# Performance work log

Hardware: AMD Instinct MI355X
Metric: run time of the kernel (lower is better)

The kernel has to match this reference:

```python
import jax, jax.numpy as jnp
import numpy as np

B, L, F = 16, 1080, 2
D = 128          # d_model
NC = 64          # num_cnn_channels
DIN = 256        # expand * d_model
N = 16           # d_state
K = 4            # d_conv
R = 8            # dt_rank = ceil(d_model/16)
OUT = 3
NB = 3           # num_mamba_blocks


def setup_inputs() -> dict:
    key = jax.random.key(0)
    ks = jax.random.split(key, 24)
    nrm = lambda k, shape, s=0.05: (jax.random.normal(k, shape) * s).astype(jnp.float32)
    bn = lambda c: jnp.stack([jnp.ones(c), jnp.zeros(c), jnp.zeros(c), jnp.ones(c)]).astype(jnp.float32)
    return {
        'x': jax.random.normal(ks[0], (B, L, F), dtype=jnp.float32),
        'emb_W': nrm(ks[1], (F, D), 0.5), 'emb_b': jnp.zeros(D, jnp.float32),
        'c3_W': nrm(ks[2], (NC, D, 3)), 'c3_b': jnp.zeros(NC, jnp.float32), 'bn3': bn(NC),
        'c5_W': nrm(ks[3], (NC, D, 5)), 'c5_b': jnp.zeros(NC, jnp.float32), 'bn5': bn(NC),
        'c7_W': nrm(ks[4], (NC, D, 7)), 'c7_b': jnp.zeros(NC, jnp.float32), 'bn7': bn(NC),
        'cf_W': nrm(ks[5], (D, 3 * NC, 1)), 'cf_b': jnp.zeros(D, jnp.float32), 'bnf': bn(D),
        'ln_g': jnp.ones((NB, D), jnp.float32), 'ln_b': jnp.zeros((NB, D), jnp.float32),
        'in_W': nrm(ks[6], (NB, 2 * DIN, D)),
        'mconv_W': nrm(ks[7], (NB, DIN, K), 0.2), 'mconv_b': jnp.zeros((NB, DIN), jnp.float32),
        'xproj_W': nrm(ks[8], (NB, R + 2 * N, DIN)),
        'dt_W': nrm(ks[9], (NB, DIN, R), 0.1), 'dt_b': jnp.full((NB, DIN), -1.0, jnp.float32),
        'A_log': jnp.tile(jnp.log(jnp.arange(1.0, N + 1.0, dtype=jnp.float32)), (NB, DIN, 1)),
        'Dp': jnp.ones((NB, DIN), jnp.float32),
        'out_W': nrm(ks[10], (NB, D, DIN)),
        'flin_W': nrm(ks[11], (D, 2 * D)), 'flin_b': jnp.zeros(D, jnp.float32),
        'fc_W': nrm(ks[12], (OUT, D)), 'fc_b': jnp.zeros(OUT, jnp.float32),
    }


def conv1d(x, W, b, pad):
    # x: (B,C,L), W: (O,C,K)
    y = jax.lax.conv_general_dilated(x, W, (1,), [(pad, pad)],
                                     dimension_numbers=('NCH', 'OIH', 'NCH'))
    return y + b[None, :, None]


def bn_relu(x, bn, eps=1e-5):
    g, b, m, v = bn  # each (C,)
    return jax.nn.relu((x - m[None, :, None]) * (g / jnp.sqrt(v + eps))[None, :, None] + b[None, :, None])


def layernorm(x, g, b, eps=1e-5):
    mu = x.mean(-1, keepdims=True)
    var = ((x - mu) ** 2).mean(-1, keepdims=True)
    return (x - mu) / jnp.sqrt(var + eps) * g + b


def pos_encoding(seq_len, d_model):
    pos = jnp.arange(seq_len, dtype=jnp.float32)[:, None]
    div = jnp.exp(jnp.arange(0, d_model, 2, dtype=jnp.float32) * (-np.log(10000.0) / d_model))
    pe = jnp.zeros((seq_len, d_model), jnp.float32)
    pe = pe.at[:, 0::2].set(jnp.sin(pos * div)).at[:, 1::2].set(jnp.cos(pos * div))
    return pe


def selective_scan(u, dt, A, Bm, Cm, Dp):
    # u,dt: (b,l,d); A: (d,n); Bm,Cm: (b,l,n); Dp: (d,)
    dA = jnp.exp(dt[..., None] * A)                    # (b,l,d,n)
    dBu = (dt * u)[..., None] * Bm[:, :, None, :]      # (b,l,d,n)

    def step(h, t):
        dA_t, dBu_t, C_t = t
        h = dA_t * h + dBu_t                           # (b,d,n)
        return h, jnp.einsum('bdn,bn->bd', h, C_t)

    h0 = jnp.zeros((u.shape[0], u.shape[2], A.shape[1]), u.dtype)
    _, ys = jax.lax.scan(step, h0, (jnp.swapaxes(dA, 0, 1), jnp.swapaxes(dBu, 0, 1), jnp.swapaxes(Cm, 0, 1)))
    return jnp.swapaxes(ys, 0, 1) + u * Dp


def mamba_block(x, in_W, conv_W, conv_b, xproj_W, dt_W, dt_b, A_log, Dp, out_W):
    xz = x @ in_W.T                                    # (b,l,2*din)
    xs, z = jnp.split(xz, 2, axis=-1)
    xc = jnp.swapaxes(xs, 1, 2)                        # (b,din,l)
    xc = jax.lax.conv_general_dilated(xc, conv_W[:, None, :], (1,), [(K - 1, 0)],
                                      dimension_numbers=('NCH', 'OIH', 'NCH'),
                                      feature_group_count=DIN)
    u = jax.nn.silu(jnp.swapaxes(xc + conv_b[None, :, None], 1, 2))  # (b,l,din)
    dbl = u @ xproj_W.T
    dt, Bm, Cm = dbl[..., :R], dbl[..., R:R + N], dbl[..., R + N:]
    dt = jax.nn.softplus(dt @ dt_W.T + dt_b)
    A = -jnp.exp(A_log)
    y = selective_scan(u, dt, A, Bm, Cm, Dp)
    return (y * jax.nn.silu(z)) @ out_W.T


def reference(x, emb_W, emb_b, c3_W, c3_b, bn3, c5_W, c5_b, bn5, c7_W, c7_b, bn7,
              cf_W, cf_b, bnf, ln_g, ln_b, in_W, mconv_W, mconv_b, xproj_W,
              dt_W, dt_b, A_log, Dp, out_W, flin_W, flin_b, fc_W, fc_b):
    xe = x @ emb_W + emb_b + pos_encoding(x.shape[1], emb_W.shape[1])  # (B,L,D)
    ci = jnp.swapaxes(xe, 1, 2)                                        # (B,D,L)
    o3 = bn_relu(conv1d(ci, c3_W, c3_b, 1), bn3)
    o5 = bn_relu(conv1d(ci, c5_W, c5_b, 2), bn5)
    o7 = bn_relu(conv1d(ci, c7_W, c7_b, 3), bn7)
    cc = jnp.concatenate([o3, o5, o7], axis=1)                         # (B,3*NC,L)
    cf = bn_relu(conv1d(cc, cf_W, cf_b, 0), bnf)
    cnn_feat = jnp.swapaxes(cf, 1, 2)                                  # (B,L,D)
    m = xe
    for i in range(NB):  # Sequential(LN, Mamba, Dropout) -- no residual, dropout=eval
        m = mamba_block(layernorm(m, ln_g[i], ln_b[i]), in_W[i], mconv_W[i], mconv_b[i],
                        xproj_W[i], dt_W[i], dt_b[i], A_log[i], Dp[i], out_W[i])
    fused = jax.nn.relu(jnp.concatenate([cnn_feat, m], axis=-1) @ flin_W.T + flin_b)
    pooled = fused.mean(axis=1)                                        # AdaptiveAvgPool1d(1)
    return pooled @ fc_W.T + fc_b
```

## Files before the change

### kernel.cpp

```cpp
#include <hip/hip_runtime.h>
#include <math.h>

#define LSEQ   1080
#define NBATCH 16
#define BLROWS (LSEQ*NBATCH)
#define CHN    27
#define LCH    40

typedef __bf16  bf16x8 __attribute__((ext_vector_type(8)));
typedef float   f32x4  __attribute__((ext_vector_type(4)));
typedef short   short8 __attribute__((ext_vector_type(8)));
typedef short   short4v __attribute__((ext_vector_type(4)));

__device__ __forceinline__ float silu_f(float x) { return x / (1.f + __expf(-x)); }

__device__ __forceinline__ unsigned short f2bf(float f) {
    unsigned int u = __float_as_uint(f);
    u += 0x7fffu + ((u >> 16) & 1u);
    return (unsigned short)(u >> 16);
}
__device__ __forceinline__ float bf2f(unsigned short h) {
    return __uint_as_float(((unsigned int)h) << 16);
}

__global__ __launch_bounds__(256) void embed_kernel(
    const float* __restrict__ x, const float* __restrict__ embW,
    const float* __restrict__ embb, float* __restrict__ xe)
{
    int idx = blockIdx.x * 256 + threadIdx.x;
    if (idx >= BLROWS * 128) return;
    int d = idx & 127;
    int r = idx >> 7;
    int t = r % LSEQ;
    float x0 = x[(size_t)r * 2], x1 = x[(size_t)r * 2 + 1];
    int i2 = d & 126;
    float div = expf((float)i2 * (-9.210340371976184f / 128.f));
    float arg = (float)t * div;
    float pe = (d & 1) ? cosf(arg) : sinf(arg);
    xe[idx] = fmaf(x0, embW[d], fmaf(x1, embW[128 + d], embb[d] + pe));
}

__global__ __launch_bounds__(256) void convw_all(
    const float* __restrict__ c3W, const float* __restrict__ c5W,
    const float* __restrict__ c7W, const float* __restrict__ cfW,
    const float* __restrict__ inW, const float* __restrict__ xpW,
    const float* __restrict__ otW, const float* __restrict__ flW,
    unsigned short* __restrict__ c3h, unsigned short* __restrict__ c3l,
    unsigned short* __restrict__ c5h, unsigned short* __restrict__ c5l,
    unsigned short* __restrict__ c7h, unsigned short* __restrict__ c7l,
    unsigned short* __restrict__ cfh, unsigned short* __restrict__ cfl,
    unsigned short* __restrict__ inh, unsigned short* __restrict__ inl,
    unsigned short* __restrict__ xph, unsigned short* __restrict__ xpl,
    unsigned short* __restrict__ oth, unsigned short* __restrict__ otl,
    unsigned short* __restrict__ flh, unsigned short* __restrict__ fll)
{
    int idx = blockIdx.x * 256 + threadIdx.x;
    float v;
    unsigned short *dh, *dl;
    int off;
    if (idx < 122880) {
        const float* src; int T;
        if (idx < 24576)      { src = c3W; T = 3; off = idx;          dh = c3h; dl = c3l; }
        else if (idx < 65536) { src = c5W; T = 5; off = idx - 24576;  dh = c5h; dl = c5l; }
        else                  { src = c7W; T = 7; off = idx - 65536;  dh = c7h; dl = c7l; }
        int kk = off % (128 * T);
        int n  = off / (128 * T);
        int tap = kk / 128, d = kk % 128;
        v = src[((size_t)n * 128 + d) * T + tap];
    } else if (idx < 147456) {
        off = idx - 122880; dh = cfh; dl = cfl; v = cfW[off];
    } else if (idx < 344064) {
        off = idx - 147456; dh = inh; dl = inl; v = inW[off];
    } else if (idx < 393216) {
        off = idx - 344064; dh = xph; dl = xpl;
        int k = off % 256;
        int n = (off / 256) % 64;
        int blk = off / (256 * 64);
        v = (n < 40) ? xpW[((size_t)blk * 40 + n) * 256 + k] : 0.f;
    } else if (idx < 491520) {
        off = idx - 393216; dh = oth; dl = otl; v = otW[off];
    } else {
        off = idx - 491520; dh = flh; dl = fll; v = flW[off];
    }
    unsigned short h = f2bf(v);
    dh[off] = h;
    dl[off] = f2bf(v - bf2f(h));
}

template<int BM, int BN>
__device__ __forceinline__ void gemm_body(
    const float* __restrict__ Ab, int lda,
    const unsigned short* __restrict__ Wh, const unsigned short* __restrict__ Wl,
    int Ntot, int Kd, int KT, int pad,
    const float* __restrict__ bias, const float* __restrict__ bn, int bnN, int epi,
    float* __restrict__ Cb, int ldc, int t0, int n0)
{
    constexpr int WM = BM / 2, WN = BN / 2;
    constexpr int MR = WM / 16, NR = WN / 16;
    constexpr int LA = (BM * 8) / 256;
    constexpr int LB = (BN * 4) / 256;

    __shared__ unsigned short Ah[BM][40], Al[BM][40];
    __shared__ unsigned short Bh[BN][40], Bl[BN][40];

    const int tid = threadIdx.x;
    const int wrow = Kd * KT;
    const int lane = tid & 63, wid = tid >> 6;
    const int wr = wid >> 1, wc = wid & 1;
    const int fr = lane & 15, fq = lane >> 4;

    f32x4 acc[MR][NR];
#pragma unroll
    for (int m = 0; m < MR; ++m)
#pragma unroll
        for (int n = 0; n < NR; ++n) acc[m][n] = (f32x4){0.f, 0.f, 0.f, 0.f};

    for (int tap = 0; tap < KT; ++tap) {
        const int shift = tap - pad;
        for (int ks = 0; ks < Kd; ks += 32) {
#pragma unroll
            for (int l = 0; l < LA; ++l) {
                int c = tid + l * 256;
                int row = c >> 3, kc = (c & 7) << 2;
                int ts = t0 + row + shift;
                float4 av = make_float4(0.f, 0.f, 0.f, 0.f);
                if (ts >= 0 && ts < LSEQ)
                    av = *(const float4*)(Ab + (size_t)ts * lda + ks + kc);
                alignas(8) unsigned short hs[4], ls[4];
                float fv[4] = {av.x, av.y, av.z, av.w};
#pragma unroll
                for (int j = 0; j < 4; ++j) {
                    unsigned short h = f2bf(fv[j]);
                    hs[j] = h;
                    ls[j] = f2bf(fv[j] - bf2f(h));
                }
                *(short4v*)&Ah[row][kc] = *(short4v*)hs;
                *(short4v*)&Al[row][kc] = *(short4v*)ls;
            }
            const int kglob = tap * Kd + ks;
#pragma unroll
            for (int l = 0; l < LB; ++l) {
                int c = tid + l * 256;
                int col = c >> 2, kc = (c & 3) << 3;
                size_t src = (size_t)(n0 + col) * wrow + kglob + kc;
                *(short8*)&Bh[col][kc] = *(const short8*)&Wh[src];
                *(short8*)&Bl[col][kc] = *(const short8*)&Wl[src];
            }
            __syncthreads();
            bf16x8 bhf[NR], blf[NR];
#pragma unroll
            for (int n = 0; n < NR; ++n) {
                int colr = wc * WN + n * 16 + fr;
                bhf[n] = __builtin_bit_cast(bf16x8, *(const short8*)&Bh[colr][fq * 8]);
                blf[n] = __builtin_bit_cast(bf16x8, *(const short8*)&Bl[colr][fq * 8]);
            }
#pragma unroll
            for (int m = 0; m < MR; ++m) {
                int rowr = wr * WM + m * 16 + fr;
                bf16x8 ahf = __builtin_bit_cast(bf16x8, *(const short8*)&Ah[rowr][fq * 8]);
                bf16x8 alf = __builtin_bit_cast(bf16x8, *(const short8*)&Al[rowr][fq * 8]);
#pragma unroll
                for (int n = 0; n < NR; ++n) {
                    acc[m][n] = __builtin_amdgcn_mfma_f32_16x16x32_bf16(ahf, bhf[n], acc[m][n], 0, 0, 0);
                    acc[m][n] = __builtin_amdgcn_mfma_f32_16x16x32_bf16(ahf, blf[n], acc[m][n], 0, 0, 0);
                    acc[m][n] = __builtin_amdgcn_mfma_f32_16x16x32_bf16(alf, bhf[n], acc[m][n], 0, 0, 0);
                }
            }
            __syncthreads();
        }
    }

#pragma unroll
    for (int m = 0; m < MR; ++m) {
#pragma unroll
        for (int n = 0; n < NR; ++n) {
            int colg = n0 + wc * WN + n * 16 + fr;
            if (colg >= Ntot) continue;
#pragma unroll
            for (int r = 0; r < 4; ++r) {
                int t = t0 + wr * WM + m * 16 + fq * 4 + r;
                if (t >= LSEQ) continue;
                float v = acc[m][n][r];
                if (epi == 1) {
                    v += bias[colg];
                    float gg = bn[colg], bb = bn[bnN + colg];
                    float mm = bn[2 * bnN + colg], vv = bn[3 * bnN + colg];
                    v = (v - mm) * (gg / sqrtf(vv + 1e-5f)) + bb;
                    v = v > 0.f ? v : 0.f;
                } else if (epi == 2) {
                    v += bias[colg];
                    v = v > 0.f ? v : 0.f;
                }
                Cb[(size_t)t * ldc + colg] = v;
            }
        }
    }
}

template<int BM, int BN>
__global__ __launch_bounds__(256) void gemm_mfma(
    const float* __restrict__ A, int lda,
    const unsigned short* __restrict__ Wh, const unsigned short* __restrict__ Wl,
    int Ntot, int Kd, int KT, int pad,
    const float* __restrict__ bias, const float* __restrict__ bn, int bnN, int epi,
    float* __restrict__ C, int ldc)
{
    const int b = blockIdx.z;
    gemm_body<BM, BN>(A + (size_t)b * LSEQ * lda, lda, Wh, Wl, Ntot, Kd, KT, pad,
                      bias, bn, bnN, epi, C + (size_t)b * LSEQ * ldc, ldc,
                      blockIdx.y * BM, blockIdx.x * BN);
}

__global__ __launch_bounds__(256) void convtri_mfma(
    const float* __restrict__ A,
    const unsigned short* __restrict__ c3h, const unsigned short* __restrict__ c3l,
    const unsigned short* __restrict__ c5h, const unsigned short* __restrict__ c5l,
    const unsigned short* __restrict__ c7h, const unsigned short* __restrict__ c7l,
    const float* __restrict__ c3b, const float* __restrict__ c5b, const float* __restrict__ c7b,
    const float* __restrict__ bn3, const float* __restrict__ bn5, const float* __restrict__ bn7,
    float* __restrict__ C)
{
    const int br = blockIdx.x;
    const int b  = blockIdx.z;
    const int KT = 3 + 2 * br, pad = 1 + br;
    const unsigned short* Wh = (br == 0) ? c3h : (br == 1) ? c5h : c7h;
    const unsigned short* Wl = (br == 0) ? c3l : (br == 1) ? c5l : c7l;
    const float* bias = (br == 0) ? c3b : (br == 1) ? c5b : c7b;
    const float* bn   = (br == 0) ? bn3 : (br == 1) ? bn5 : bn7;
    gemm_body<64, 64>(A + (size_t)b * LSEQ * 128, 128, Wh, Wl, 64, 128, KT, pad,
                      bias, bn, 64, 1,
                      C + (size_t)b * LSEQ * 192 + br * 64, 192,
                      blockIdx.y * 64, 0);
}

__global__ __launch_bounds__(256) void ln_kernel(
    const float* __restrict__ in, const float* __restrict__ g,
    const float* __restrict__ b2, float* __restrict__ out)
{
    int lane = threadIdx.x & 63;
    int wid  = threadIdx.x >> 6;
    int row = blockIdx.x * 4 + wid;
    if (row >= BLROWS) return;
    const float* rp = in + (size_t)row * 128;
    float v0 = rp[lane], v1 = rp[lane + 64];
    float s = v0 + v1;
#pragma unroll
    for (int o2 = 32; o2 > 0; o2 >>= 1) s += __shfl_xor(s, o2, 64);
    float mu = s * (1.f / 128.f);
    float d0 = v0 - mu, d1 = v1 - mu;
    float q = d0 * d0 + d1 * d1;
#pragma unroll
    for (int o2 = 32; o2 > 0; o2 >>= 1) q += __shfl_xor(q, o2, 64);
    float rs = 1.f / sqrtf(q * (1.f / 128.f) + 1e-5f);
    float* op = out + (size_t)row * 128;
    op[lane]      = d0 * rs * g[lane]      + b2[lane];
    op[lane + 64] = d1 * rs * g[lane + 64] + b2[lane + 64];
}

__global__ __launch_bounds__(256) void mconv_kernel(
    const float* __restrict__ xz, const float* __restrict__ Wc,
    const float* __restrict__ bc, float* __restrict__ u)
{
    int idx = blockIdx.x * 256 + threadIdx.x;
    int c = idx & 255;
    int r = idx >> 8;
    if (r >= BLROWS) return;
    int t = r % LSEQ;
    const float* xs = xz + (size_t)r * 512 + c;
    float acc = bc[c];
    if (t >= 3) acc = fmaf(xs[-3 * 512], Wc[c * 4 + 0], acc);
    if (t >= 2) acc = fmaf(xs[-2 * 512], Wc[c * 4 + 1], acc);
    if (t >= 1) acc = fmaf(xs[-1 * 512], Wc[c * 4 + 2], acc);
    acc = fmaf(xs[0], Wc[c * 4 + 3], acc);
    u[(size_t)r * 256 + c] = silu_f(acc);
}

__global__ __launch_bounds__(256) void dtk_kernel(
    const float* __restrict__ dbl, const float* __restrict__ dtW,
    const float* __restrict__ dtb, float* __restrict__ dtout)
{
    int idx = blockIdx.x * 256 + threadIdx.x;
    int c = idx & 255;
    int r = idx >> 8;
    if (r >= BLROWS) return;
    const float* dr = dbl + (size_t)r * 40;
    float a = dtb[c];
#pragma unroll
    for (int j = 0; j < 8; ++j) a = fmaf(dr[j], dtW[c * 8 + j], a);
    float sp = (a > 20.f) ? a : log1pf(__expf(a));
    dtout[(size_t)r * 256 + c] = sp;
}

__global__ __launch_bounds__(256) void scan1_kernel(
    const float* __restrict__ dt, const float* __restrict__ u,
    const float* __restrict__ dbl, const float* __restrict__ Alog,
    float* __restrict__ P, float* __restrict__ S)
{
    int idx = blockIdx.x * 256 + threadIdx.x;
    int ng = idx & 3;
    int d  = (idx >> 2) & 255;
    int rest = idx >> 10;
    int ch = rest % CHN;
    int b  = rest / CHN;
    int n0 = ng * 4;
    float A2[4];
#pragma unroll
    for (int j = 0; j < 4; ++j) A2[j] = -__expf(Alog[d * 16 + n0 + j]);
    float p[4] = {1.f, 1.f, 1.f, 1.f}, s[4] = {0.f, 0.f, 0.f, 0.f};
    int r0 = b * LSEQ + ch * LCH;
    for (int q = 0; q < LCH; ++q) {
        size_t r = (size_t)(r0 + q);
        float dtv = dt[r * 256 + d];
        float uv  = u [r * 256 + d];
        float dtu = dtv * uv;
        float4 Br = *(const float4*)(dbl + r * 40 + 8 + n0);
        float bv[4] = {Br.x, Br.y, Br.z, Br.w};
#pragma unroll
        for (int j = 0; j < 4; ++j) {
            float a = __expf(dtv * A2[j]);
            p[j] *= a;
            s[j] = fmaf(a, s[j], dtu * bv[j]);
        }
    }
    size_t ob = ((size_t)(b * CHN + ch) * 256 + d) * 16 + n0;
    *(float4*)&P[ob] = make_float4(p[0], p[1], p[2], p[3]);
    *(float4*)&S[ob] = make_float4(s[0], s[1], s[2], s[3]);
}

__global__ __launch_bounds__(256) void scan2_kernel(
    const float* __restrict__ P, const float* __restrict__ S, float* __restrict__ H0)
{
    int idx = blockIdx.x * 256 + threadIdx.x;
    int n = idx & 15;
    int d = (idx >> 4) & 255;
    int b = idx >> 12;
    float h = 0.f;
    for (int ch = 0; ch < CHN; ++ch) {
        size_t o = ((size_t)(b * CHN + ch) * 256 + d) * 16 + n;
        H0[o] = h;
        h = fmaf(P[o], h, S[o]);
    }
}

__global__ __launch_bounds__(256) void scan3_kernel(
    const float* __restrict__ dt, const float* __restrict__ u,
    const float* __restrict__ dbl, const float* __restrict__ Alog,
    const float* __restrict__ H0, const float* __restrict__ Dp,
    const float* __restrict__ xz, float* __restrict__ g)
{
    int idx = blockIdx.x * 256 + threadIdx.x;
    int ng = idx & 3;
    int d  = (idx >> 2) & 255;
    int rest = idx >> 10;
    int ch = rest % CHN;
    int b  = rest / CHN;
    int n0 = ng * 4;
    float A2[4];
#pragma unroll
    for (int j = 0; j < 4; ++j) A2[j] = -__expf(Alog[d * 16 + n0 + j]);
    size_t ob = ((size_t)(b * CHN + ch) * 256 + d) * 16 + n0;
    float4 h4 = *(const float4*)&H0[ob];
    float h[4] = {h4.x, h4.y, h4.z, h4.w};
    float Dpd = Dp[d];
    int r0 = b * LSEQ + ch * LCH;
    for (int q = 0; q < LCH; ++q) {
        size_t r = (size_t)(r0 + q);
        float dtv = dt[r * 256 + d];
        float uv  = u [r * 256 + d];
        float dtu = dtv * uv;
        float4 Br = *(const float4*)(dbl + r * 40 + 8 + n0);
        float4 Cr = *(const float4*)(dbl + r * 40 + 24 + n0);
        float bv[4] = {Br.x, Br.y, Br.z, Br.w};
        float cv[4] = {Cr.x, Cr.y, Cr.z, Cr.w};
        float pacc = 0.f;
#pragma unroll
        for (int j = 0; j < 4; ++j) {
            float a = __expf(dtv * A2[j]);
            h[j] = fmaf(a, h[j], dtu * bv[j]);
            pacc = fmaf(h[j], cv[j], pacc);
        }
        float acc = pacc + __shfl_xor(pacc, 1);
        acc += __shfl_xor(acc, 2);
        if (ng == 0) {
            float yv = fmaf(uv, Dpd, acc);
            float zv = xz[r * 512 + 256 + d];
            g[r * 256 + d] = yv * silu_f(zv);
        }
    }
}

__global__ __launch_bounds__(128) void pool1_kernel(
    const float* __restrict__ fused, float* __restrict__ part)
{
    int d = threadIdx.x;
    int blk = blockIdx.x;
    int ch = blk % CHN;
    int b  = blk / CHN;
    int t0 = ch * LCH;
    float s = 0.f;
    for (int q = 0; q < LCH; ++q)
        s += fused[((size_t)(b * LSEQ + t0 + q)) * 128 + d];
    part[(size_t)(b * CHN + ch) * 128 + d] = s;
}

__global__ __launch_bounds__(128) void pool2_kernel(
    const float* __restrict__ part, const float* __restrict__ fcW,
    const float* __restrict__ fcb, float* __restrict__ out)
{
    __shared__ float pl[128];
    int d = threadIdx.x;
    int b = blockIdx.x;
    float s = 0.f;
    for (int ch = 0; ch < CHN; ++ch) s += part[(size_t)(b * CHN + ch) * 128 + d];
    pl[d] = s * (1.f / 1080.f);
    __syncthreads();
    if (d < 3) {
        float a = fcb[d];
        for (int dd = 0; dd < 128; ++dd) a = fmaf(pl[dd], fcW[d * 128 + dd], a);
        out[b * 3 + d] = a;
    }
}

extern "C" void kernel_launch(void* const* d_in, const int* in_sizes, int n_in,
                              void* d_out, int out_size, void* d_ws, size_t ws_size,
                              hipStream_t stream)
{
    const float* x    = (const float*)d_in[0];
    const float* embW = (const float*)d_in[1];
    const float* embb = (const float*)d_in[2];
    const float* c3W  = (const float*)d_in[3];
    const float* c3b  = (const float*)d_in[4];
    const float* bn3  = (const float*)d_in[5];
    const float* c5W  = (const float*)d_in[6];
    const float* c5b  = (const float*)d_in[7];
    const float* bn5  = (const float*)d_in[8];
    const float* c7W  = (const float*)d_in[9];
    const float* c7b  = (const float*)d_in[10];
    const float* bn7  = (const float*)d_in[11];
    const float* cfW  = (const float*)d_in[12];
    const float* cfb  = (const float*)d_in[13];
    const float* bnf  = (const float*)d_in[14];
    const float* lng  = (const float*)d_in[15];
    const float* lnb  = (const float*)d_in[16];
    const float* inW  = (const float*)d_in[17];
    const float* mcW  = (const float*)d_in[18];
    const float* mcb  = (const float*)d_in[19];
    const float* xpW  = (const float*)d_in[20];
    const float* dtW  = (const float*)d_in[21];
    const float* dtbp = (const float*)d_in[22];
    const float* Alog = (const float*)d_in[23];
    const float* Dp   = (const float*)d_in[24];
    const float* outW = (const float*)d_in[25];
    const float* flW  = (const float*)d_in[26];
    const float* flb  = (const float*)d_in[27];
    const float* fcW  = (const float*)d_in[28];
    const float* fcb  = (const float*)d_in[29];

    float* ws = (float*)d_ws;
    size_t off = 0;
    auto alloc = [&](size_t n) { float* p = ws + off; off += n; return p; };
    float* xe   = alloc((size_t)BLROWS * 128);
    float* lnx  = alloc((size_t)BLROWS * 128);
    float* xz   = alloc((size_t)BLROWS * 512);
    float* ub   = alloc((size_t)BLROWS * 256);
    float* dtt  = alloc((size_t)BLROWS * 256);
    float* dbl  = alloc((size_t)BLROWS * 40);
    float* gb   = alloc((size_t)BLROWS * 256);
    float* mbuf = alloc((size_t)BLROWS * 128);
    float* fin  = alloc((size_t)BLROWS * 256);
    float* Pb   = alloc((size_t)NBATCH * CHN * 256 * 16);
    float* Sb   = alloc((size_t)NBATCH * CHN * 256 * 16);
    float* h0b  = alloc((size_t)NBATCH * CHN * 256 * 16);
    float* cc    = gb;
    float* fused = lnx;

    off = (off + 3) & ~(size_t)3;
    unsigned short* us = (unsigned short*)(ws + off);
    size_t uo = 0;
    auto ualloc = [&](size_t n) { unsigned short* p = us + uo; uo += n; return p; };
    unsigned short* c3h = ualloc(64 * 384);  unsigned short* c3l = ualloc(64 * 384);
    unsigned short* c5h = ualloc(64 * 640);  unsigned short* c5l = ualloc(64 * 640);
    unsigned short* c7h = ualloc(64 * 896);  unsigned short* c7l = ualloc(64 * 896);
    unsigned short* cfh = ualloc(128 * 192); unsigned short* cfl = ualloc(128 * 192);
    unsigned short* inh = ualloc((size_t)1536 * 128); unsigned short* inl = ualloc((size_t)1536 * 128);
    unsigned short* xph = ualloc((size_t)3 * 64 * 256); unsigned short* xpl = ualloc((size_t)3 * 64 * 256);
    unsigned short* oth = ualloc((size_t)384 * 256); unsigned short* otl = ualloc((size_t)384 * 256);
    unsigned short* flh = ualloc((size_t)128 * 256); unsigned short* fll = ualloc((size_t)128 * 256);
    (void)ws_size; (void)in_sizes; (void)n_in; (void)out_size;

    convw_all<<<2048, 256, 0, stream>>>(c3W, c5W, c7W, cfW, inW, xpW, outW, flW,
                                        c3h, c3l, c5h, c5l, c7h, c7l, cfh, cfl,
                                        inh, inl, xph, xpl, oth, otl, flh, fll);

    embed_kernel<<<(BLROWS * 128) / 256, 256, 0, stream>>>(x, embW, embb, xe);

    dim3 gtri(3, 17, NBATCH);
    convtri_mfma<<<gtri, 256, 0, stream>>>(xe, c3h, c3l, c5h, c5l, c7h, c7l,
                                           c3b, c5b, c7b, bn3, bn5, bn7, cc);
    dim3 g64(1, 17, NBATCH);
    dim3 g128(1, 17, NBATCH);
    gemm_mfma<64, 128><<<g128, 256, 0, stream>>>(cc, 192, cfh, cfl, 128, 192, 1, 0,
                                                 cfb, bnf, 128, 1, fin, 256);

    for (int i = 0; i < 3; ++i) {
        const float* min_ = (i == 0) ? xe : ((i == 1) ? mbuf : xe);
        float* mout = (i == 0) ? mbuf : ((i == 1) ? xe : (fin + 128));
        int ldout = (i < 2) ? 128 : 256;

        ln_kernel<<<BLROWS / 4, 256, 0, stream>>>(min_, lng + i * 128, lnb + i * 128, lnx);

        dim3 gin(4, 17, NBATCH);
        gemm_mfma<64, 128><<<gin, 256, 0, stream>>>(lnx, 128, inh + (size_t)i * 512 * 128,
                                                    inl + (size_t)i * 512 * 128,
                                                    512, 128, 1, 0, nullptr, nullptr, 0, 0,
                                                    xz, 512);

        mconv_kernel<<<BLROWS, 256, 0, stream>>>(xz, mcW + i * 256 * 4, mcb + i * 256, ub);

        gemm_mfma<64, 64><<<g64, 256, 0, stream>>>(ub, 256, xph + (size_t)i * 64 * 256,
                                                   xpl + (size_t)i * 64 * 256,
                                                   40, 256, 1, 0, nullptr, nullptr, 0, 0,
                                                   dbl, 40);

        dtk_kernel<<<BLROWS, 256, 0, stream>>>(dbl, dtW + i * 256 * 8, dtbp + i * 256, dtt);

        scan1_kernel<<<(NBATCH * CHN * 1024) / 256, 256, 0, stream>>>(
            dtt, ub, dbl, Alog + i * 256 * 16, Pb, Sb);
        scan2_kernel<<<(NBATCH * 256 * 16) / 256, 256, 0, stream>>>(Pb, Sb, h0b);
        scan3_kernel<<<(NBATCH * CHN * 1024) / 256, 256, 0, stream>>>(
            dtt, ub, dbl, Alog + i * 256 * 16, h0b, Dp + i * 256, xz, gb);

        gemm_mfma<64, 128><<<g128, 256, 0, stream>>>(gb, 256, oth + (size_t)i * 128 * 256,
                                                     otl + (size_t)i * 128 * 256,
                                                     128, 256, 1, 0, nullptr, nullptr, 0, 0,
                                                     mout, ldout);
    }

    gemm_mfma<64, 128><<<g128, 256, 0, stream>>>(fin, 256, flh, fll, 128, 256, 1, 0,
                                                 flb, nullptr, 0, 2, fused, 128);

    pool1_kernel<<<NBATCH * CHN, 128, 0, stream>>>(fused, Pb);
    pool2_kernel<<<NBATCH, 128, 0, stream>>>(Pb, fcW, fcb, (float*)d_out);
}
```

Before: 682.0 us.

## Pre-split activations to bf16 hi/lo in producers and unify tri-conv GEMM

Producer kernels (conv epilogue, LN, mconv, scan3, out-proj) now write bf16 hi/lo pairs directly, so consumer GEMMs load pre-split halves instead of converting fp32 on every tile load. The three conv branches are merged into one 192-column GEMM over a shared 7-tap halo tile. BN scale and shift are precomputed once into a small table. The in-proj GEMM uses a larger 128x128 tile, and buffers are reorganised. The cost is extra writes of two half arrays per activation, plus zero-padded taps that add MFMA work for the k3 and k5 branches.

Result: no change. 680.4 us (-0.2%).

```diff
diff --git a/kernel.cpp b/kernel.cpp
--- a/kernel.cpp
+++ b/kernel.cpp
@@ -21,6 +21,10 @@
 }
 __device__ __forceinline__ float bf2f(unsigned short h) {
     return __uint_as_float(((unsigned int)h) << 16);
+}
+__device__ __forceinline__ void split_bf(float v, unsigned short& h, unsigned short& l) {
+    h = f2bf(v);
+    l = f2bf(v - bf2f(h));
 }
 
 __global__ __launch_bounds__(256) void embed_kernel(
@@ -40,136 +44,264 @@
     xe[idx] = fmaf(x0, embW[d], fmaf(x1, embW[128 + d], embb[d] + pe));
 }
 
+#define JOB_W192  172032
+#define JOB_CF    196608
+#define JOB_IN    393216
+#define JOB_XP    442368
+#define JOB_OT    540672
+#define JOB_FL    573440
+#define JOB_END   574080
 __global__ __launch_bounds__(256) void convw_all(
     const float* __restrict__ c3W, const float* __restrict__ c5W,
     const float* __restrict__ c7W, const float* __restrict__ cfW,
     const float* __restrict__ inW, const float* __restrict__ xpW,
     const float* __restrict__ otW, const float* __restrict__ flW,
-    unsigned short* __restrict__ c3h, unsigned short* __restrict__ c3l,
-    unsigned short* __restrict__ c5h, unsigned short* __restrict__ c5l,
-    unsigned short* __restrict__ c7h, unsigned short* __restrict__ c7l,
+    const float* __restrict__ c3b, const float* __restrict__ c5b, const float* __restrict__ c7b,
+    const float* __restrict__ bn3, const float* __restrict__ bn5, const float* __restrict__ bn7,
+    const float* __restrict__ cfb, const float* __restrict__ bnf,
+    unsigned short* __restrict__ w192h, unsigned short* __restrict__ w192l,
     unsigned short* __restrict__ cfh, unsigned short* __restrict__ cfl,
     unsigned short* __restrict__ inh, unsigned short* __restrict__ inl,
     unsigned short* __restrict__ xph, unsigned short* __restrict__ xpl,
     unsigned short* __restrict__ oth, unsigned short* __restrict__ otl,
-    unsigned short* __restrict__ flh, unsigned short* __restrict__ fll)
+    unsigned short* __restrict__ flh, unsigned short* __restrict__ fll,
+    float* __restrict__ schpack)
 {
     int idx = blockIdx.x * 256 + threadIdx.x;
+    if (idx >= JOB_END) return;
+    if (idx >= JOB_FL + 32768) { return; }
     float v;
     unsigned short *dh, *dl;
     int off;
-    if (idx < 122880) {
-        const float* src; int T;
-        if (idx < 24576)      { src = c3W; T = 3; off = idx;          dh = c3h; dl = c3l; }
-        else if (idx < 65536) { src = c5W; T = 5; off = idx - 24576;  dh = c5h; dl = c5l; }
-        else                  { src = c7W; T = 7; off = idx - 65536;  dh = c7h; dl = c7l; }
-        int kk = off % (128 * T);
-        int n  = off / (128 * T);
-        int tap = kk / 128, d = kk % 128;
-        v = src[((size_t)n * 128 + d) * T + tap];
-    } else if (idx < 147456) {
-        off = idx - 122880; dh = cfh; dl = cfl; v = cfW[off];
-    } else if (idx < 344064) {
-        off = idx - 147456; dh = inh; dl = inl; v = inW[off];
-    } else if (idx < 393216) {
-        off = idx - 344064; dh = xph; dl = xpl;
-        int k = off % 256;
-        int n = (off / 256) % 64;
-        int blk = off / (256 * 64);
+    if (idx < JOB_W192) {
+        off = idx;
+        int n = off / 896, kk = off % 896;
+        int slot = kk >> 7, d = kk & 127;
+        int br = n >> 6, c = n & 63;
+        int KT = 3 + 2 * br, pad = 1 + br;
+        int tp = slot - 3 + pad;
+        const float* w = (br == 0) ? c3W : (br == 1) ? c5W : c7W;
+        v = (tp >= 0 && tp < KT) ? w[((c << 7) + d) * KT + tp] : 0.f;
+        dh = w192h; dl = w192l;
+    } else if (idx < JOB_CF) {
+        off = idx - JOB_W192; v = cfW[off]; dh = cfh; dl = cfl;
+    } else if (idx < JOB_IN) {
+        off = idx - JOB_CF; v = inW[off]; dh = inh; dl = inl;
+    } else if (idx < JOB_XP) {
+        off = idx - JOB_IN;
+        int k = off & 255, n = (off >> 8) & 63, blk = off >> 14;
         v = (n < 40) ? xpW[((size_t)blk * 40 + n) * 256 + k] : 0.f;
-    } else if (idx < 491520) {
-        off = idx - 393216; dh = oth; dl = otl; v = otW[off];
+        dh = xph; dl = xpl;
+    } else if (idx < JOB_OT) {
+        off = idx - JOB_XP; v = otW[off]; dh = oth; dl = otl;
+    } else if (idx < JOB_FL) {
+        off = idx - JOB_OT; v = flW[off]; dh = flh; dl = fll;
     } else {
-        off = idx - 491520; dh = flh; dl = fll; v = flW[off];
-    }
-    unsigned short h = f2bf(v);
-    dh[off] = h;
-    dl[off] = f2bf(v - bf2f(h));
-}
-
-template<int BM, int BN>
-__device__ __forceinline__ void gemm_body(
-    const float* __restrict__ Ab, int lda,
+        int j = idx - JOB_FL;
+        if (j < 384) {
+            int col = (j < 192) ? j : j - 192;
+            int isSh = j >= 192;
+            int br = col >> 6, c = col & 63;
+            const float* bn = (br == 0) ? bn3 : (br == 1) ? bn5 : bn7;
+            float bias = ((br == 0) ? c3b : (br == 1) ? c5b : c7b)[c];
+            float g = bn[c], bb = bn[64 + c], m = bn[128 + c], vv = bn[192 + c];
+            float scale = g * rsqrtf(vv + 1e-5f);
+            float shift = (bias - m) * scale + bb;
+            schpack[j] = isSh ? shift : scale;
+        } else {
+            int j2 = j - 384;
+            int col = j2 & 127;
+            int isSh = j2 >= 128;
+            float g = bnf[col], bb = bnf[128 + col], m = bnf[256 + col], vv = bnf[384 + col];
+            float scale = g * rsqrtf(vv + 1e-5f);
+            float shift = (cfb[col] - m) * scale + bb;
+            schpack[384 + j2] = isSh ? shift : scale;
+        }
+        return;
+    }
+    unsigned short h, l;
+    split_bf(v, h, l);
+    dh[off] = h; dl[off] = l;
+}
+
+__global__ __launch_bounds__(256) void gemm_conv(
+    const float* __restrict__ xe,
     const unsigned short* __restrict__ Wh, const unsigned short* __restrict__ Wl,
-    int Ntot, int Kd, int KT, int pad,
-    const float* __restrict__ bias, const float* __restrict__ bn, int bnN, int epi,
-    float* __restrict__ Cb, int ldc, int t0, int n0)
-{
-    constexpr int WM = BM / 2, WN = BN / 2;
-    constexpr int MR = WM / 16, NR = WN / 16;
-    constexpr int LA = (BM * 8) / 256;
-    constexpr int LB = (BN * 4) / 256;
-
-    __shared__ unsigned short Ah[BM][40], Al[BM][40];
-    __shared__ unsigned short Bh[BN][40], Bl[BN][40];
-
+    const float* __restrict__ sc, const float* __restrict__ sh,
+    unsigned short* __restrict__ Ch, unsigned short* __restrict__ Cl)
+{
+    __shared__ unsigned short Ah[70][40], Al[70][40];
+    __shared__ unsigned short Bh[64][136], Bl[64][136];
     const int tid = threadIdx.x;
-    const int wrow = Kd * KT;
+    const int n0 = blockIdx.x * 64, t0 = blockIdx.y * 64, b = blockIdx.z;
+    const float* Ab = xe + (size_t)b * LSEQ * 128;
     const int lane = tid & 63, wid = tid >> 6;
     const int wr = wid >> 1, wc = wid & 1;
     const int fr = lane & 15, fq = lane >> 4;
-
-    f32x4 acc[MR][NR];
-#pragma unroll
-    for (int m = 0; m < MR; ++m)
-#pragma unroll
-        for (int n = 0; n < NR; ++n) acc[m][n] = (f32x4){0.f, 0.f, 0.f, 0.f};
-
-    for (int tap = 0; tap < KT; ++tap) {
-        const int shift = tap - pad;
-        for (int ks = 0; ks < Kd; ks += 32) {
-#pragma unroll
-            for (int l = 0; l < LA; ++l) {
-                int c = tid + l * 256;
-                int row = c >> 3, kc = (c & 7) << 2;
-                int ts = t0 + row + shift;
+    f32x4 acc[2][2];
+#pragma unroll
+    for (int m = 0; m < 2; ++m)
+#pragma unroll
+        for (int n = 0; n < 2; ++n) acc[m][n] = (f32x4){0.f, 0.f, 0.f, 0.f};
+
+    for (int ks = 0; ks < 128; ks += 32) {
+#pragma unroll
+        for (int l = 0; l < 3; ++l) {
+            int c = tid + l * 256;
+            if (c < 560) {
+                int row = c >> 3, kq = (c & 7) << 2;
+                int ts = t0 - 3 + row;
                 float4 av = make_float4(0.f, 0.f, 0.f, 0.f);
                 if (ts >= 0 && ts < LSEQ)
-                    av = *(const float4*)(Ab + (size_t)ts * lda + ks + kc);
+                    av = *(const float4*)(Ab + (size_t)ts * 128 + ks + kq);
                 alignas(8) unsigned short hs[4], ls[4];
                 float fv[4] = {av.x, av.y, av.z, av.w};
 #pragma unroll
-                for (int j = 0; j < 4; ++j) {
-                    unsigned short h = f2bf(fv[j]);
-                    hs[j] = h;
-                    ls[j] = f2bf(fv[j] - bf2f(h));
-                }
-                *(short4v*)&Ah[row][kc] = *(short4v*)hs;
-                *(short4v*)&Al[row][kc] = *(short4v*)ls;
+                for (int j = 0; j < 4; ++j) split_bf(fv[j], hs[j], ls[j]);
+                *(short4v*)&Ah[row][kq] = *(short4v*)hs;
+                *(short4v*)&Al[row][kq] = *(short4v*)ls;
             }
-            const int kglob = tap * Kd + ks;
-#pragma unroll
-            for (int l = 0; l < LB; ++l) {
+        }
+        for (int g = 0; g < 2; ++g) {
+            const int ntap = (g == 0) ? 4 : 3;
+#pragma unroll
+            for (int l = 0; l < 4; ++l) {
                 int c = tid + l * 256;
-                int col = c >> 2, kc = (c & 3) << 3;
-                size_t src = (size_t)(n0 + col) * wrow + kglob + kc;
-                *(short8*)&Bh[col][kc] = *(const short8*)&Wh[src];
-                *(short8*)&Bl[col][kc] = *(const short8*)&Wl[src];
-            }
-            __syncthreads();
-            bf16x8 bhf[NR], blf[NR];
-#pragma unroll
-            for (int n = 0; n < NR; ++n) {
-                int colr = wc * WN + n * 16 + fr;
-                bhf[n] = __builtin_bit_cast(bf16x8, *(const short8*)&Bh[colr][fq * 8]);
-                blf[n] = __builtin_bit_cast(bf16x8, *(const short8*)&Bl[colr][fq * 8]);
-            }
-#pragma unroll
-            for (int m = 0; m < MR; ++m) {
-                int rowr = wr * WM + m * 16 + fr;
-                bf16x8 ahf = __builtin_bit_cast(bf16x8, *(const short8*)&Ah[rowr][fq * 8]);
-                bf16x8 alf = __builtin_bit_cast(bf16x8, *(const short8*)&Al[rowr][fq * 8]);
-#pragma unroll
-                for (int n = 0; n < NR; ++n) {
-                    acc[m][n] = __builtin_amdgcn_mfma_f32_16x16x32_bf16(ahf, bhf[n], acc[m][n], 0, 0, 0);
-                    acc[m][n] = __builtin_amdgcn_mfma_f32_16x16x32_bf16(ahf, blf[n], acc[m][n], 0, 0, 0);
-                    acc[m][n] = __builtin_amdgcn_mfma_f32_16x16x32_bf16(alf, bhf[n], acc[m][n], 0, 0, 0);
+                int col = c >> 4, rem = c & 15, tt = rem >> 2, kq = (rem & 3) << 3;
+                if (tt < ntap) {
+                    int tap = g * 4 + tt;
+                    size_t s = (size_t)(n0 + col) * 896 + tap * 128 + ks + kq;
+                    *(short8*)&Bh[col][tt * 32 + kq] = *(const short8*)&Wh[s];
+                    *(short8*)&Bl[col][tt * 32 + kq] = *(const short8*)&Wl[s];
                 }
             }
             __syncthreads();
-        }
-    }
-
+            for (int tt = 0; tt < ntap; ++tt) {
+                int tap = g * 4 + tt;
+                bf16x8 bhf[2], blf[2];
+#pragma unroll
+                for (int n = 0; n < 2; ++n) {
+                    int col = wc * 32 + n * 16 + fr;
+                    bhf[n] = __builtin_bit_cast(bf16x8, *(const short8*)&Bh[col][tt * 32 + fq * 8]);
+                    blf[n] = __builtin_bit_cast(bf16x8, *(const short8*)&Bl[col][tt * 32 + fq * 8]);
+                }
+#pragma unroll
+                for (int m = 0; m < 2; ++m) {
+                    int rowA = wr * 32 + m * 16 + fr + tap;
+                    bf16x8 ahf = __builtin_bit_cast(bf16x8, *(const short8*)&Ah[rowA][fq * 8]);
+                    bf16x8 alf = __builtin_bit_cast(bf16x8, *(const short8*)&Al[rowA][fq * 8]);
+#pragma unroll
+                    for (int n = 0; n < 2; ++n) {
+                        acc[m][n] = __builtin_amdgcn_mfma_f32_16x16x32_bf16(ahf, bhf[n], acc[m][n], 0, 0, 0);
+                        acc[m][n] = __builtin_amdgcn_mfma_f32_16x16x32_bf16(ahf, blf[n], acc[m][n], 0, 0, 0);
+                        acc[m][n] = __builtin_amdgcn_mfma_f32_16x16x32_bf16(alf, bhf[n], acc[m][n], 0, 0, 0);
+                    }
+                }
+            }
+            __syncthreads();
+        }
+    }
+    unsigned short* Chb = Ch + (size_t)b * LSEQ * 192;
+    unsigned short* Clb = Cl + (size_t)b * LSEQ * 192;
+#pragma unroll
+    for (int m = 0; m < 2; ++m) {
+#pragma unroll
+        for (int n = 0; n < 2; ++n) {
+            int colg = n0 + wc * 32 + n * 16 + fr;
+            float scl = sc[colg], shf2 = sh[colg];
+#pragma unroll
+            for (int r = 0; r < 4; ++r) {
+                int t = t0 + wr * 32 + m * 16 + fq * 4 + r;
+                if (t >= LSEQ) continue;
+                float v = fmaf(acc[m][n][r], scl, shf2);
+                v = v > 0.f ? v : 0.f;
+                unsigned short h, l;
+                split_bf(v, h, l);
+                Chb[(size_t)t * 192 + colg] = h;
+                Clb[(size_t)t * 192 + colg] = l;
+            }
+        }
+    }
+}
+
+template<int BM, int BN>
+__global__ __launch_bounds__(256) void gemm_plain(
+    const unsigned short* __restrict__ Aph, const unsigned short* __restrict__ Apl, int lda,
+    const unsigned short* __restrict__ Wh, const unsigned short* __restrict__ Wl, int Kd,
+    int Ntot, int epi,
+    const float* __restrict__ sc, const float* __restrict__ sh, const float* __restrict__ bias,
+    float* __restrict__ Cf, int ldc,
+    unsigned short* __restrict__ Ch, unsigned short* __restrict__ Cl, int ldch)
+{
+    constexpr int WM = BM / 2, WN = BN / 2;
+    constexpr int MR = WM / 16, NR = WN / 16;
+    constexpr int ACH = (BM * 4) / 256;
+    constexpr int BCH = (BN * 4) / 256;
+    __shared__ unsigned short Ah[BM][40], Al[BM][40];
+    __shared__ unsigned short Bh[BN][40], Bl[BN][40];
+    const int tid = threadIdx.x;
+    const int b = blockIdx.z, t0 = blockIdx.y * BM, n0 = blockIdx.x * BN;
+    const unsigned short* Abh = Aph + (size_t)b * LSEQ * lda;
+    const unsigned short* Abl = Apl + (size_t)b * LSEQ * lda;
+    const int lane = tid & 63, wid = tid >> 6;
+    const int wr = wid >> 1, wc = wid & 1;
+    const int fr = lane & 15, fq = lane >> 4;
+    f32x4 acc[MR][NR];
+#pragma unroll
+    for (int m = 0; m < MR; ++m)
+#pragma unroll
+        for (int n = 0; n < NR; ++n) acc[m][n] = (f32x4){0.f, 0.f, 0.f, 0.f};
+
+    const short8 zz = {0, 0, 0, 0, 0, 0, 0, 0};
+    for (int ks = 0; ks < Kd; ks += 32) {
+#pragma unroll
+        for (int l = 0; l < ACH; ++l) {
+            int c = tid + l * 256;
+            int row = c >> 2, kc = (c & 3) << 3;
+            int t = t0 + row;
+            short8 vh = zz, vl = zz;
+            if (t < LSEQ) {
+                size_t s = (size_t)t * lda + ks + kc;
+                vh = *(const short8*)&Abh[s];
+                vl = *(const short8*)&Abl[s];
+            }
+            *(short8*)&Ah[row][kc] = vh;
+            *(short8*)&Al[row][kc] = vl;
+        }
+#pragma unroll
+        for (int l = 0; l < BCH; ++l) {
+            int c = tid + l * 256;
+            int col = c >> 2, kc = (c & 3) << 3;
+            size_t s = (size_t)(n0 + col) * Kd + ks + kc;
+            *(short8*)&Bh[col][kc] = *(const short8*)&Wh[s];
+            *(short8*)&Bl[col][kc] = *(const short8*)&Wl[s];
+        }
+        __syncthreads();
+        bf16x8 bhf[NR], blf[NR];
+#pragma unroll
+        for (int n = 0; n < NR; ++n) {
+            int col = wc * WN + n * 16 + fr;
+            bhf[n] = __builtin_bit_cast(bf16x8, *(const short8*)&Bh[col][fq * 8]);
+            blf[n] = __builtin_bit_cast(bf16x8, *(const short8*)&Bl[col][fq * 8]);
+        }
+#pragma unroll
+        for (int m = 0; m < MR; ++m) {
+            int rowr = wr * WM + m * 16 + fr;
+            bf16x8 ahf = __builtin_bit_cast(bf16x8, *(const short8*)&Ah[rowr][fq * 8]);
+            bf16x8 alf = __builtin_bit_cast(bf16x8, *(const short8*)&Al[rowr][fq * 8]);
+#pragma unroll
+            for (int n = 0; n < NR; ++n) {
+                acc[m][n] = __builtin_amdgcn_mfma_f32_16x16x32_bf16(ahf, bhf[n], acc[m][n], 0, 0, 0);
+                acc[m][n] = __builtin_amdgcn_mfma_f32_16x16x32_bf16(ahf, blf[n], acc[m][n], 0, 0, 0);
+                acc[m][n] = __builtin_amdgcn_mfma_f32_16x16x32_bf16(alf, bhf[n], acc[m][n], 0, 0, 0);
+            }
+        }
+        __syncthreads();
+    }
+
+    float* Cfb = Cf ? Cf + (size_t)b * LSEQ * ldc : nullptr;
+    unsigned short* Chb = Ch ? Ch + (size_t)b * LSEQ * ldch : nullptr;
+    unsigned short* Clb = Cl ? Cl + (size_t)b * LSEQ * ldch : nullptr;
 #pragma unroll
     for (int m = 0; m < MR; ++m) {
 #pragma unroll
@@ -181,61 +313,34 @@
                 int t = t0 + wr * WM + m * 16 + fq * 4 + r;
                 if (t >= LSEQ) continue;
                 float v = acc[m][n][r];
-                if (epi == 1) {
-                    v += bias[colg];
-                    float gg = bn[colg], bb = bn[bnN + colg];
-                    float mm = bn[2 * bnN + colg], vv = bn[3 * bnN + colg];
-                    v = (v - mm) * (gg / sqrtf(vv + 1e-5f)) + bb;
+                if (epi == 0) {
+                    Cfb[(size_t)t * ldc + colg] = v;
+                } else if (epi == 1) {
+                    v = fmaf(v, sc[colg], sh[colg]);
                     v = v > 0.f ? v : 0.f;
+                    unsigned short h, l;
+                    split_bf(v, h, l);
+                    Chb[(size_t)t * ldch + colg] = h;
+                    Clb[(size_t)t * ldch + colg] = l;
                 } else if (epi == 2) {
                     v += bias[colg];
                     v = v > 0.f ? v : 0.f;
+                    Cfb[(size_t)t * ldc + colg] = v;
+                } else {
+                    unsigned short h, l;
+                    split_bf(v, h, l);
+                    Chb[(size_t)t * ldch + colg] = h;
+                    Clb[(size_t)t * ldch + colg] = l;
                 }
-                Cb[(size_t)t * ldc + colg] = v;
             }
         }
     }
-}
-
-template<int BM, int BN>
-__global__ __launch_bounds__(256) void gemm_mfma(
-    const float* __restrict__ A, int lda,
-    const unsigned short* __restrict__ Wh, const unsigned short* __restrict__ Wl,
-    int Ntot, int Kd, int KT, int pad,
-    const float* __restrict__ bias, const float* __restrict__ bn, int bnN, int epi,
-    float* __restrict__ C, int ldc)
-{
-    const int b = blockIdx.z;
-    gemm_body<BM, BN>(A + (size_t)b * LSEQ * lda, lda, Wh, Wl, Ntot, Kd, KT, pad,
-                      bias, bn, bnN, epi, C + (size_t)b * LSEQ * ldc, ldc,
-                      blockIdx.y * BM, blockIdx.x * BN);
-}
-
-__global__ __launch_bounds__(256) void convtri_mfma(
-    const float* __restrict__ A,
-    const unsigned short* __restrict__ c3h, const unsigned short* __restrict__ c3l,
-    const unsigned short* __restrict__ c5h, const unsigned short* __restrict__ c5l,
-    const unsigned short* __restrict__ c7h, const unsigned short* __restrict__ c7l,
-    const float* __restrict__ c3b, const float* __restrict__ c5b, const float* __restrict__ c7b,
-    const float* __restrict__ bn3, const float* __restrict__ bn5, const float* __restrict__ bn7,
-    float* __restrict__ C)
-{
-    const int br = blockIdx.x;
-    const int b  = blockIdx.z;
-    const int KT = 3 + 2 * br, pad = 1 + br;
-    const unsigned short* Wh = (br == 0) ? c3h : (br == 1) ? c5h : c7h;
-    const unsigned short* Wl = (br == 0) ? c3l : (br == 1) ? c5l : c7l;
-    const float* bias = (br == 0) ? c3b : (br == 1) ? c5b : c7b;
-    const float* bn   = (br == 0) ? bn3 : (br == 1) ? bn5 : bn7;
-    gemm_body<64, 64>(A + (size_t)b * LSEQ * 128, 128, Wh, Wl, 64, 128, KT, pad,
-                      bias, bn, 64, 1,
-                      C + (size_t)b * LSEQ * 192 + br * 64, 192,
-                      blockIdx.y * 64, 0);
 }
 
 __global__ __launch_bounds__(256) void ln_kernel(
     const float* __restrict__ in, const float* __restrict__ g,
-    const float* __restrict__ b2, float* __restrict__ out)
+    const float* __restrict__ b2, unsigned short* __restrict__ oh,
+    unsigned short* __restrict__ ol)
 {
     int lane = threadIdx.x & 63;
     int wid  = threadIdx.x >> 6;
@@ -252,14 +357,18 @@
 #pragma unroll
     for (int o2 = 32; o2 > 0; o2 >>= 1) q += __shfl_xor(q, o2, 64);
     float rs = 1.f / sqrtf(q * (1.f / 128.f) + 1e-5f);
-    float* op = out + (size_t)row * 128;
-    op[lane]      = d0 * rs * g[lane]      + b2[lane];
-    op[lane + 64] = d1 * rs * g[lane + 64] + b2[lane + 64];
+    float y0 = d0 * rs * g[lane]      + b2[lane];
+    float y1 = d1 * rs * g[lane + 64] + b2[lane + 64];
+    unsigned short h, l;
+    size_t o = (size_t)row * 128;
+    split_bf(y0, h, l); oh[o + lane] = h;      ol[o + lane] = l;
+    split_bf(y1, h, l); oh[o + lane + 64] = h; ol[o + lane + 64] = l;
 }
 
 __global__ __launch_bounds__(256) void mconv_kernel(
     const float* __restrict__ xz, const float* __restrict__ Wc,
-    const float* __restrict__ bc, float* __restrict__ u)
+    const float* __restrict__ bc, float* __restrict__ u,
+    unsigned short* __restrict__ uh, unsigned short* __restrict__ ul)
 {
     int idx = blockIdx.x * 256 + threadIdx.x;
     int c = idx & 255;
@@ -272,7 +381,12 @@
     if (t >= 2) acc = fmaf(xs[-2 * 512], Wc[c * 4 + 1], acc);
     if (t >= 1) acc = fmaf(xs[-1 * 512], Wc[c * 4 + 2], acc);
     acc = fmaf(xs[0], Wc[c * 4 + 3], acc);
-    u[(size_t)r * 256 + c] = silu_f(acc);
+    float uv = silu_f(acc);
+    size_t o = (size_t)r * 256 + c;
+    u[o] = uv;
+    unsigned short h, l;
+    split_bf(uv, h, l);
+    uh[o] = h; ul[o] = l;
 }
 
 __global__ __launch_bounds__(256) void dtk_kernel(
@@ -346,7 +460,8 @@
     const float* __restrict__ dt, const float* __restrict__ u,
     const float* __restrict__ dbl, const float* __restrict__ Alog,
     const float* __restrict__ H0, const float* __restrict__ Dp,
-    const float* __restrict__ xz, float* __restrict__ g)
+    const float* __restrict__ xz, unsigned short* __restrict__ gh,
+    unsigned short* __restrict__ gl)
 {
     int idx = blockIdx.x * 256 + threadIdx.x;
     int ng = idx & 3;
@@ -384,7 +499,11 @@
         if (ng == 0) {
             float yv = fmaf(uv, Dpd, acc);
             float zv = xz[r * 512 + 256 + d];
-            g[r * 256 + d] = yv * silu_f(zv);
+            float gv = yv * silu_f(zv);
+            unsigned short hh, ll;
+            split_bf(gv, hh, ll);
+            gh[r * 256 + d] = hh;
+            gl[r * 256 + d] = ll;
         }
     }
 }
@@ -460,67 +579,68 @@
     size_t off = 0;
     auto alloc = [&](size_t n) { float* p = ws + off; off += n; return p; };
     float* xe   = alloc((size_t)BLROWS * 128);
-    float* lnx  = alloc((size_t)BLROWS * 128);
     float* xz   = alloc((size_t)BLROWS * 512);
     float* ub   = alloc((size_t)BLROWS * 256);
     float* dtt  = alloc((size_t)BLROWS * 256);
     float* dbl  = alloc((size_t)BLROWS * 40);
-    float* gb   = alloc((size_t)BLROWS * 256);
-    float* mbuf = alloc((size_t)BLROWS * 128);
-    float* fin  = alloc((size_t)BLROWS * 256);
     float* Pb   = alloc((size_t)NBATCH * CHN * 256 * 16);
     float* Sb   = alloc((size_t)NBATCH * CHN * 256 * 16);
     float* h0b  = alloc((size_t)NBATCH * CHN * 256 * 16);
-    float* cc    = gb;
-    float* fused = lnx;
+    float* schpack = alloc(640);
+    float* fused = xz;
+    float* mtail = xz + (size_t)BLROWS * 384;
 
     off = (off + 3) & ~(size_t)3;
     unsigned short* us = (unsigned short*)(ws + off);
     size_t uo = 0;
     auto ualloc = [&](size_t n) { unsigned short* p = us + uo; uo += n; return p; };
-    unsigned short* c3h = ualloc(64 * 384);  unsigned short* c3l = ualloc(64 * 384);
-    unsigned short* c5h = ualloc(64 * 640);  unsigned short* c5l = ualloc(64 * 640);
-    unsigned short* c7h = ualloc(64 * 896);  unsigned short* c7l = ualloc(64 * 896);
+    unsigned short* cch  = ualloc((size_t)BLROWS * 192);
+    unsigned short* ccl  = ualloc((size_t)BLROWS * 192);
+    unsigned short* finh = ualloc((size_t)BLROWS * 256);
+    unsigned short* finl = ualloc((size_t)BLROWS * 256);
+    unsigned short* ubh  = ualloc((size_t)BLROWS * 256);
+    unsigned short* ubl  = ualloc((size_t)BLROWS * 256);
+    unsigned short* w192h = ualloc((size_t)192 * 896); unsigned short* w192l = ualloc((size_t)192 * 896);
     unsigned short* cfh = ualloc(128 * 192); unsigned short* cfl = ualloc(128 * 192);
     unsigned short* inh = ualloc((size_t)1536 * 128); unsigned short* inl = ualloc((size_t)1536 * 128);
     unsigned short* xph = ualloc((size_t)3 * 64 * 256); unsigned short* xpl = ualloc((size_t)3 * 64 * 256);
     unsigned short* oth = ualloc((size_t)384 * 256); unsigned short* otl = ualloc((size_t)384 * 256);
     unsigned short* flh = ualloc((size_t)128 * 256); unsigned short* fll = ualloc((size_t)128 * 256);
+    unsigned short* lnxh = cch;
+    unsigned short* lnxl = ccl;
+    unsigned short* gbh  = ubh;
+    unsigned short* gbl  = ubl;
     (void)ws_size; (void)in_sizes; (void)n_in; (void)out_size;
 
-    convw_all<<<2048, 256, 0, stream>>>(c3W, c5W, c7W, cfW, inW, xpW, outW, flW,
-                                        c3h, c3l, c5h, c5l, c7h, c7l, cfh, cfl,
-                                        inh, inl, xph, xpl, oth, otl, flh, fll);
+    convw_all<<<(JOB_END + 255) / 256, 256, 0, stream>>>(
+        c3W, c5W, c7W, cfW, inW, xpW, outW, flW,
+        c3b, c5b, c7b, bn3, bn5, bn7, cfb, bnf,
+        w192h, w192l, cfh, cfl, inh, inl, xph, xpl, oth, otl, flh, fll, schpack);
 
     embed_kernel<<<(BLROWS * 128) / 256, 256, 0, stream>>>(x, embW, embb, xe);
 
-    dim3 gtri(3, 17, NBATCH);
-    convtri_mfma<<<gtri, 256, 0, stream>>>(xe, c3h, c3l, c5h, c5l, c7h, c7l,
-                                           c3b, c5b, c7b, bn3, bn5, bn7, cc);
-    dim3 g64(1, 17, NBATCH);
-    dim3 g128(1, 17, NBATCH);
-    gemm_mfma<64, 128><<<g128, 256, 0, stream>>>(cc, 192, cfh, cfl, 128, 192, 1, 0,
-                                                 cfb, bnf, 128, 1, fin, 256);
+    dim3 gconv(3, 17, NBATCH);
+    gemm_conv<<<gconv, 256, 0, stream>>>(xe, w192h, w192l, schpack, schpack + 192, cch, ccl);
+    dim3 g17(1, 17, NBATCH);
+    gemm_plain<64, 128><<<g17, 256, 0, stream>>>(
+        cch, ccl, 192, cfh, cfl, 192, 128, 1,
+        schpack + 384, schpack + 512, nullptr, nullptr, 0, finh, finl, 256);
 
     for (int i = 0; i < 3; ++i) {
-        const float* min_ = (i == 0) ? xe : ((i == 1) ? mbuf : xe);
-        float* mout = (i == 0) ? mbuf : ((i == 1) ? xe : (fin + 128));
-        int ldout = (i < 2) ? 128 : 256;
-
-        ln_kernel<<<BLROWS / 4, 256, 0, stream>>>(min_, lng + i * 128, lnb + i * 128, lnx);
-
-        dim3 gin(4, 17, NBATCH);
-        gemm_mfma<64, 128><<<gin, 256, 0, stream>>>(lnx, 128, inh + (size_t)i * 512 * 128,
-                                                    inl + (size_t)i * 512 * 128,
-                                                    512, 128, 1, 0, nullptr, nullptr, 0, 0,
-                                                    xz, 512);
-
-        mconv_kernel<<<BLROWS, 256, 0, stream>>>(xz, mcW + i * 256 * 4, mcb + i * 256, ub);
-
-        gemm_mfma<64, 64><<<g64, 256, 0, stream>>>(ub, 256, xph + (size_t)i * 64 * 256,
-                                                   xpl + (size_t)i * 64 * 256,
-                                                   40, 256, 1, 0, nullptr, nullptr, 0, 0,
-                                                   dbl, 40);
+        const float* min_ = (i == 0) ? xe : mtail;
+
+        ln_kernel<<<BLROWS / 4, 256, 0, stream>>>(min_, lng + i * 128, lnb + i * 128, lnxh, lnxl);
+
+        dim3 gin(4, 9, NBATCH);
+        gemm_plain<128, 128><<<gin, 256, 0, stream>>>(
+            lnxh, lnxl, 128, inh + (size_t)i * 512 * 128, inl + (size_t)i * 512 * 128, 128,
+            512, 0, nullptr, nullptr, nullptr, xz, 512, nullptr, nullptr, 0);
+
+        mconv_kernel<<<BLROWS, 256, 0, stream>>>(xz, mcW + i * 256 * 4, mcb + i * 256, ub, ubh, ubl);
+
+        gemm_plain<64, 64><<<g17, 256, 0, stream>>>(
+            ubh, ubl, 256, xph + (size_t)i * 64 * 256, xpl + (size_t)i * 64 * 256, 256,
+            40, 0, nullptr, nullptr, nullptr, dbl, 40, nullptr, nullptr, 0);
 
         dtk_kernel<<<BLROWS, 256, 0, stream>>>(dbl, dtW + i * 256 * 8, dtbp + i * 256, dtt);
 
@@ -528,16 +648,22 @@
             dtt, ub, dbl, Alog + i * 256 * 16, Pb, Sb);
         scan2_kernel<<<(NBATCH * 256 * 16) / 256, 256, 0, stream>>>(Pb, Sb, h0b);
         scan3_kernel<<<(NBATCH * CHN * 1024) / 256, 256, 0, stream>>>(
-            dtt, ub, dbl, Alog + i * 256 * 16, h0b, Dp + i * 256, xz, gb);
-
-        gemm_mfma<64, 128><<<g128, 256, 0, stream>>>(gb, 256, oth + (size_t)i * 128 * 256,
-                                                     otl + (size_t)i * 128 * 256,
-                                                     128, 256, 1, 0, nullptr, nullptr, 0, 0,
-                                                     mout, ldout);
-    }
-
-    gemm_mfma<64, 128><<<g128, 256, 0, stream>>>(fin, 256, flh, fll, 128, 256, 1, 0,
-                                                 flb, nullptr, 0, 2, fused, 128);
+            dtt, ub, dbl, Alog + i * 256 * 16, h0b, Dp + i * 256, xz, gbh, gbl);
+
+        if (i < 2) {
+            gemm_plain<64, 128><<<g17, 256, 0, stream>>>(
+                gbh, gbl, 256, oth + (size_t)i * 128 * 256, otl + (size_t)i * 128 * 256, 256,
+                128, 0, nullptr, nullptr, nullptr, mtail, 128, nullptr, nullptr, 0);
+        } else {
+            gemm_plain<64, 128><<<g17, 256, 0, stream>>>(
+                gbh, gbl, 256, oth + (size_t)i * 128 * 256, otl + (size_t)i * 128 * 256, 256,
+                128, 3, nullptr, nullptr, nullptr, nullptr, 0, finh + 128, finl + 128, 256);
+        }
+    }
+
+    gemm_plain<64, 128><<<g17, 256, 0, stream>>>(
+        finh, finl, 256, flh, fll, 256, 128, 2,
+        nullptr, nullptr, flb, fused, 128, nullptr, nullptr, 0);
 
     pool1_kernel<<<NBATCH * CHN, 128, 0, stream>>>(fused, Pb);
     pool2_kernel<<<NBATCH, 128, 0, stream>>>(Pb, fcW, fcb, (float*)d_out);
```
